# Optimization experiments

Measured on AMD Instinct MI355X. Metric: run time of the kernel, lower is better.

## Reference

```python
import jax, jax.numpy as jnp
import numpy as np

NEG = -1000000000.0

def _gat(x, adj_pos, W, a_src, a_dst):
    # x: [N,F], W: [H,F], a_src/a_dst: [1,H]
    h = x @ W.T                                          # [N,H]
    e = jax.nn.leaky_relu(h @ a_src.T + (h @ a_dst.T).T, 0.2)  # [N,N] additive attn
    e = jnp.where(adj_pos, e, NEG)
    alpha = jax.nn.softmax(e, axis=-1)
    return alpha @ h                                     # [N,H]

def setup_inputs() -> dict:
    key = jax.random.key(0)
    ks = jax.random.split(key, 24)
    N, F, Cf, C, H = 4096, 64, 10, 64, 128
    s = 0.05
    nrm = lambda k, shp: (jax.random.normal(k, shp, jnp.float32) * s)
    return dict(
        node_features=jax.random.normal(ks[0], (N, F), jnp.float32),
        candidate_features=jax.random.uniform(ks[1], (N, C, Cf), dtype=jnp.float32),
        adjacency=jax.random.randint(ks[2], (N, N), 0, 2).astype(jnp.int32),
        action_mask=jax.random.uniform(ks[3], (N, C), dtype=jnp.float32),
        W1=nrm(ks[4], (H, F)), a1s=nrm(ks[5], (1, H)), a1d=nrm(ks[6], (1, H)),
        W2=nrm(ks[7], (H, H)), a2s=nrm(ks[8], (1, H)), a2d=nrm(ks[9], (1, H)),
        ln_w=jnp.ones((H,), jnp.float32), ln_b=jnp.zeros((H,), jnp.float32),
        Wc1=nrm(ks[10], (H, Cf)), bc1=jnp.zeros((H,), jnp.float32),
        Wc2=nrm(ks[11], (H, H)), bc2=jnp.zeros((H,), jnp.float32),
        Wq=nrm(ks[12], (H, H)), bq=jnp.zeros((H,), jnp.float32),
        Ws1=nrm(ks[13], (H, 2 * H)), bs1=jnp.zeros((H,), jnp.float32),
        Ws2=nrm(ks[14], (1, H)), bs2=jnp.zeros((1,), jnp.float32),
    )

def reference(node_features, candidate_features, adjacency, action_mask,
              W1, a1s, a1d, W2, a2s, a2d, ln_w, ln_b,
              Wc1, bc1, Wc2, bc2, Wq, bq, Ws1, bs1, Ws2, bs2):
    gelu = lambda x: jax.nn.gelu(x, approximate=False)  # torch nn.GELU default (erf)
    adj_pos = adjacency > 0
    # two GAT layers with residual + LayerNorm
    h = jax.nn.relu(_gat(node_features, adj_pos, W1, a1s, a1d))      # [N,H]
    h = jax.nn.relu(_gat(h, adj_pos, W2, a2s, a2d)) + h
    mu = jnp.mean(h, axis=-1, keepdims=True)
    var = jnp.var(h, axis=-1, keepdims=True)
    h = (h - mu) * jax.lax.rsqrt(var + 1e-5) * ln_w + ln_b           # LayerNorm
    # candidate encoder
    cand = gelu(candidate_features @ Wc1.T + bc1)                    # [N,C,H]
    cand = gelu(cand @ Wc2.T + bc2)
    q = (h @ Wq.T + bq)[:, None, :]                                  # [N,1,H]
    fused = jnp.concatenate([q * cand, cand], axis=-1)               # [N,C,2H]
    logits = (gelu(fused @ Ws1.T + bs1) @ Ws2.T + bs2)[..., 0]       # [N,C]
    cf = candidate_features
    bias = (20.0 * cf[..., 0] + 4.0 * cf[..., 4] + 1.5 * cf[..., 5]
            + 1.5 * cf[..., 1] - 1.5 * cf[..., 2]
            + 1.2 * cf[..., 6] + 2.5 * cf[..., 7]
            + 1.6 * cf[..., 8] + 1.2 * cf[..., 9])
    logits = logits + bias
    # rows with no valid action: force action 0 valid
    no_valid = jnp.sum(action_mask, axis=-1) <= 0
    am = action_mask.at[:, 0].set(jnp.where(no_valid, 1.0, action_mask[:, 0]))
    return jnp.where(am > 0, logits, NEG)
```

## Files before the change

### kernel.cpp

```cpp
#include <hip/hip_runtime.h>
#include <hip/hip_bf16.h>
#include <math.h>

#define NN 4096
#define HD 128
#define NCAND 64
#define NCF 10
#define NSEG 16
#define NEGV (-1000000000.0f)

typedef __attribute__((ext_vector_type(8))) short short8_t;
typedef __attribute__((ext_vector_type(4))) float f32x4_t;

__device__ __forceinline__ short f2bf(float f) {
    union { __hip_bfloat16 h; short s; } v;
    v.h = __float2bfloat16(f);
    return v.s;
}
__device__ __forceinline__ float bf2f(short s) {
    union { unsigned u; float f; } v; v.u = ((unsigned)(unsigned short)s) << 16;
    return v.f;
}
__device__ __forceinline__ unsigned pk2(float a, float b) {
    union { __hip_bfloat162 h; unsigned u; } v;
    v.h = __float22bfloat162_rn(make_float2(a, b));
    return v.u;
}

__device__ __forceinline__ float gelu_f(float x) {
    float e = __builtin_amdgcn_exp2f(2.455466f * x);
    float r = __builtin_amdgcn_rcpf(e + 1.0f);
    return x - x * r;
}

__global__ __launch_bounds__(256) void prep_gatin_k(
    const int* __restrict__ adj, const float* __restrict__ Wc1,
    const float* __restrict__ Wc2, const float* __restrict__ Ws1,
    unsigned* __restrict__ adjb, short* __restrict__ Wc1b,
    short* __restrict__ Wc2b, short* __restrict__ Wfu,
    const float* __restrict__ X, const float* __restrict__ W1,
    const float* __restrict__ a_s, const float* __restrict__ a_d,
    float* __restrict__ sdv, short* __restrict__ Htb)
{
    constexpr int K = 64, AS = 68;
    __shared__ float in_s[16*AS];
    __shared__ float H_s[16*132];
    int tid = threadIdx.x;

    if (blockIdx.x < 2048) {
        long g = (long)blockIdx.x * 256 + tid;
        const int4* p = (const int4*)adj + g * 8;
        unsigned wd = 0;
        #pragma unroll
        for (int e = 0; e < 8; ++e) {
            int4 v = p[e];
            wd |= (unsigned)(v.x != 0) << (e*4 + 0);
            wd |= (unsigned)(v.y != 0) << (e*4 + 1);
            wd |= (unsigned)(v.z != 0) << (e*4 + 2);
            wd |= (unsigned)(v.w != 0) << (e*4 + 3);
        }
        adjb[g] = wd;
        return;
    }
    if (blockIdx.x < 2056) {
        int g = (blockIdx.x - 2048) * 256 + tid;
        const int tot = 8 * 256;
        for (int e = g; e < 128*32; e += tot) {
            int t = e >> 5, k = e & 31;
            Wc1b[e] = (k < NCF) ? f2bf(Wc1[t*NCF + k]) : (short)0;
        }
        for (int e = g; e < 128*128; e += tot) {
            int h = e >> 7, pos = e & 127;
            int n = (pos >> 3) | ((pos & 7) << 4);
            Wc2b[e] = f2bf(Wc2[h*128 + n]);
        }
        for (int e = g; e < 128*256; e += tot) {
            int h = e >> 8, j = e & 255;
            int pos = j & 127;
            int n = (pos >> 3) | ((pos & 7) << 4);
            float v = (j < 128) ? Ws1[h*256 + 128 + n] : Ws1[h*256 + n];
            Wfu[e] = f2bf(v);
        }
        return;
    }

    int n0 = (blockIdx.x - 2056) * 16;
    {
        constexpr int NV = 16*K/4;
        for (int idx = tid; idx < NV; idx += 256) {
            int row = idx / (K/4), c4 = idx - row*(K/4);
            *(float4*)&in_s[row*AS + c4*4] = *(const float4*)&X[(long)(n0+row)*K + c4*4];
        }
    }
    __syncthreads();

    int w = tid >> 6, l = tid & 63, l15 = l & 15, qd = l >> 4;
    f32x4_t acc[2];
    acc[0] = (f32x4_t){0.f,0.f,0.f,0.f};
    acc[1] = (f32x4_t){0.f,0.f,0.f,0.f};
    #pragma unroll
    for (int kc = 0; kc < K/32; ++kc) {
        int k0 = kc*32 + qd*8;
        float4 x = *(const float4*)&in_s[l15*AS + k0];
        float4 y = *(const float4*)&in_s[l15*AS + k0 + 4];
        union { short8_t s; unsigned u[4]; } a;
        a.u[0]=pk2(x.x,x.y); a.u[1]=pk2(x.z,x.w);
        a.u[2]=pk2(y.x,y.y); a.u[3]=pk2(y.z,y.w);
        #pragma unroll
        for (int it = 0; it < 2; ++it) {
            int n = (w*2+it)*16 + l15;
            float4 w0 = *(const float4*)&W1[(long)n*K + k0];
            float4 w1 = *(const float4*)&W1[(long)n*K + k0 + 4];
            union { short8_t s; unsigned u[4]; } b;
            b.u[0]=pk2(w0.x,w0.y); b.u[1]=pk2(w0.z,w0.w);
            b.u[2]=pk2(w1.x,w1.y); b.u[3]=pk2(w1.z,w1.w);
            acc[it] = __builtin_amdgcn_mfma_f32_16x16x32_bf16(a.s, b.s, acc[it], 0,0,0);
        }
    }
    #pragma unroll
    for (int it = 0; it < 2; ++it)
        #pragma unroll
        for (int r = 0; r < 4; ++r)
            H_s[(qd*4+r)*132 + (w*2+it)*16 + l15] = acc[it][r];
    __syncthreads();
    {
        int row = tid >> 4, sg = tid & 15;
        int h0 = sg*8;
        float4 as0 = *(const float4*)&a_s[h0];
        float4 as1 = *(const float4*)&a_s[h0+4];
        float4 ad0 = *(const float4*)&a_d[h0];
        float4 ad1 = *(const float4*)&a_d[h0+4];
        float hv[8];
        #pragma unroll
        for (int e = 0; e < 8; ++e) hv[e] = H_s[row*132 + h0 + e];
        float sp = hv[0]*as0.x + hv[1]*as0.y + hv[2]*as0.z + hv[3]*as0.w
                 + hv[4]*as1.x + hv[5]*as1.y + hv[6]*as1.z + hv[7]*as1.w;
        float dp = hv[0]*ad0.x + hv[1]*ad0.y + hv[2]*ad0.z + hv[3]*ad0.w
                 + hv[4]*ad1.x + hv[5]*ad1.y + hv[6]*ad1.z + hv[7]*ad1.w;
        sp += __shfl_xor(sp,1); sp += __shfl_xor(sp,2);
        sp += __shfl_xor(sp,4); sp += __shfl_xor(sp,8);
        dp += __shfl_xor(dp,1); dp += __shfl_xor(dp,2);
        dp += __shfl_xor(dp,4); dp += __shfl_xor(dp,8);
        if (sg == 0) { sdv[n0+row] = sp; sdv[NN + n0 + row] = dp; }
    }
    {
        int h = tid & 127, pr = tid >> 7;
        unsigned u[4];
        #pragma unroll
        for (int c2 = 0; c2 < 4; ++c2)
            u[c2] = pk2(H_s[(pr*8 + 2*c2)*132 + h], H_s[(pr*8 + 2*c2 + 1)*132 + h]);
        *(uint4*)&Htb[(long)h*NN + n0 + pr*8] = make_uint4(u[0],u[1],u[2],u[3]);
    }
}

template<int K, int IN, int OUT>
__global__ __launch_bounds__(256) void gatin_k3(
    const float* __restrict__ in, const float* __restrict__ Wf,
    const float* __restrict__ nump, const float* __restrict__ denp,
    float* __restrict__ G1, const float* __restrict__ ln_w,
    const float* __restrict__ ln_b,
    const float* __restrict__ a_s, const float* __restrict__ a_d,
    float* __restrict__ sdv, short* __restrict__ Htb,
    const float* __restrict__ bias, float* __restrict__ outq)
{
    constexpr int AS = K + 4;
    __shared__ float in_s[16*AS];
    __shared__ float H_s[16*132];
    int tid = threadIdx.x;
    int n0 = blockIdx.x * 16;

    if (IN == 0) {
        constexpr int NV = 16*K/4;
        for (int idx = tid; idx < NV; idx += 256) {
            int row = idx / (K/4), c4 = idx - row*(K/4);
            *(float4*)&in_s[row*AS + c4*4] = *(const float4*)&in[(long)(n0+row)*K + c4*4];
        }
    } else {
        int row = tid >> 4, c8 = (tid & 15) * 8;
        float v[8];
        #pragma unroll
        for (int i = 0; i < 8; ++i) v[i] = 0.f;
        float den = 0.f;
        const float* npr = nump + (long)(n0 + row)*NSEG*HD + c8;
        const float* dpr = denp + (long)(n0 + row)*NSEG;
        #pragma unroll
        for (int s = 0; s < NSEG; ++s) {
            const float* np = npr + s*HD;
            float4 a0 = *(const float4*)np;
            float4 a1 = *(const float4*)(np + 4);
            v[0]+=a0.x; v[1]+=a0.y; v[2]+=a0.z; v[3]+=a0.w;
            v[4]+=a1.x; v[5]+=a1.y; v[6]+=a1.z; v[7]+=a1.w;
            den += dpr[s];
        }
        float rd = (den > 0.f) ? __builtin_amdgcn_rcpf(den) : 0.f;
        if (den > 0.f) rd = rd * (2.0f - den * rd);
        #pragma unroll
        for (int i = 0; i < 8; ++i) v[i] = fmaxf(v[i]*rd, 0.f);
        if (IN == 1) {
            float4 o0 = make_float4(v[0],v[1],v[2],v[3]);
            float4 o1 = make_float4(v[4],v[5],v[6],v[7]);
            *(float4*)&G1[(long)(n0+row)*HD + c8]     = o0;
            *(float4*)&G1[(long)(n0+row)*HD + c8 + 4] = o1;
        }
        #pragma unroll
        for (int i = 0; i < 8; ++i) in_s[row*AS + c8 + i] = v[i];
    }
    __syncthreads();

    int w = tid >> 6, l = tid & 63, l15 = l & 15, qd = l >> 4;
    f32x4_t acc[2];
    acc[0] = (f32x4_t){0.f,0.f,0.f,0.f};
    acc[1] = (f32x4_t){0.f,0.f,0.f,0.f};
    #pragma unroll
    for (int kc = 0; kc < K/32; ++kc) {
        int k0 = kc*32 + qd*8;
        float4 x = *(const float4*)&in_s[l15*AS + k0];
        float4 y = *(const float4*)&in_s[l15*AS + k0 + 4];
        union { short8_t s; unsigned u[4]; } a;
        a.u[0]=pk2(x.x,x.y); a.u[1]=pk2(x.z,x.w);
        a.u[2]=pk2(y.x,y.y); a.u[3]=pk2(y.z,y.w);
        #pragma unroll
        for (int it = 0; it < 2; ++it) {
            int n = (w*2+it)*16 + l15;
            float4 w0 = *(const float4*)&Wf[(long)n*K + k0];
            float4 w1 = *(const float4*)&Wf[(long)n*K + k0 + 4];
            union { short8_t s; unsigned u[4]; } b;
            b.u[0]=pk2(w0.x,w0.y); b.u[1]=pk2(w0.z,w0.w);
            b.u[2]=pk2(w1.x,w1.y); b.u[3]=pk2(w1.z,w1.w);
            acc[it] = __builtin_amdgcn_mfma_f32_16x16x32_bf16(a.s, b.s, acc[it], 0,0,0);
        }
    }

    #pragma unroll
    for (int it = 0; it < 2; ++it)
        #pragma unroll
        for (int r = 0; r < 4; ++r)
            H_s[(qd*4+r)*132 + (w*2+it)*16 + l15] = acc[it][r];
    __syncthreads();
    {
        int row = tid >> 4, sg = tid & 15;
        int h0 = sg*8;
        float4 as0 = *(const float4*)&a_s[h0];
        float4 as1 = *(const float4*)&a_s[h0+4];
        float4 ad0 = *(const float4*)&a_d[h0];
        float4 ad1 = *(const float4*)&a_d[h0+4];
        float hv[8];
        #pragma unroll
        for (int e = 0; e < 8; ++e) hv[e] = H_s[row*132 + h0 + e];
        float sp = hv[0]*as0.x + hv[1]*as0.y + hv[2]*as0.z + hv[3]*as0.w
                 + hv[4]*as1.x + hv[5]*as1.y + hv[6]*as1.z + hv[7]*as1.w;
        float dp = hv[0]*ad0.x + hv[1]*ad0.y + hv[2]*ad0.z + hv[3]*ad0.w
                 + hv[4]*ad1.x + hv[5]*ad1.y + hv[6]*ad1.z + hv[7]*ad1.w;
        sp += __shfl_xor(sp,1); sp += __shfl_xor(sp,2);
        sp += __shfl_xor(sp,4); sp += __shfl_xor(sp,8);
        dp += __shfl_xor(dp,1); dp += __shfl_xor(dp,2);
        dp += __shfl_xor(dp,4); dp += __shfl_xor(dp,8);
        if (sg == 0) { sdv[n0+row] = sp; sdv[NN + n0 + row] = dp; }
    }
    {
        int h = tid & 127, pr = tid >> 7;
        unsigned u[4];
        #pragma unroll
        for (int c2 = 0; c2 < 4; ++c2)
            u[c2] = pk2(H_s[(pr*8 + 2*c2)*132 + h], H_s[(pr*8 + 2*c2 + 1)*132 + h]);
        *(uint4*)&Htb[(long)h*NN + n0 + pr*8] = make_uint4(u[0],u[1],u[2],u[3]);
    }
}

__global__ __launch_bounds__(256, 4) void agg_k5(
    const unsigned* __restrict__ adjb, const float* __restrict__ sdv,
    const short* __restrict__ Htb, float* __restrict__ num_part,
    float* __restrict__ den_part)
{
    __shared__ __align__(16) short Bs[128*72];
    __shared__ float dj_s[256];
    int tid = threadIdx.x;
    int i0 = blockIdx.x * 32;
    int seg = blockIdx.y;
    int w = tid >> 6, l = tid & 63, l15 = l & 15, qd = l >> 4;
    int mh = w >> 1, nh = w & 1;
    int arow = i0 + mh*16 + l15;
    float si = sdv[arow];
    const float C1 = 1.44269504f;
    const float C2 = 0.28853901f;

    dj_s[tid] = sdv[NN + seg*256 + tid];

    unsigned wbuf[8];
    {
        const uint4* ap = (const uint4*)&adjb[(long)arow*128 + seg*8];
        uint4 q0 = ap[0], q1 = ap[1];
        wbuf[0]=q0.x; wbuf[1]=q0.y; wbuf[2]=q0.z; wbuf[3]=q0.w;
        wbuf[4]=q1.x; wbuf[5]=q1.y; wbuf[6]=q1.z; wbuf[7]=q1.w;
    }

    int sh = tid >> 1, sj = (tid & 1) * 32;
    const short* srcb = Htb + (long)sh*NN + seg*256 + sj;

    f32x4_t acc[4];
    #pragma unroll
    for (int nt = 0; nt < 4; ++nt) acc[nt] = (f32x4_t){0.f,0.f,0.f,0.f};
    float den = 0.f;

    for (int c4 = 0; c4 < 4; ++c4) {
        __syncthreads();
        {
            const uint4* src = (const uint4*)(srcb + c4*64);
            uint4 v0 = src[0], v1 = src[1], v2 = src[2], v3 = src[3];
            uint4* dst = (uint4*)&Bs[sh*72 + sj];
            dst[0]=v0; dst[1]=v1; dst[2]=v2; dst[3]=v3;
        }
        __syncthreads();
        #pragma unroll
        for (int kc = 0; kc < 2; ++kc) {
            int jl = c4*64 + kc*32 + qd*8;
            float4 da = *(const float4*)&dj_s[jl];
            float4 db = *(const float4*)&dj_s[jl+4];
            unsigned byte_ = (wbuf[c4*2+kc] >> (qd*8)) & 0xffu;
            float dv[8] = {da.x,da.y,da.z,da.w,db.x,db.y,db.z,db.w};
            float v[8];
            #pragma unroll
            for (int e = 0; e < 8; ++e) {
                float z = si + dv[e];
                float k = (z > 0.f) ? C1 : C2;
                float wv = __builtin_amdgcn_exp2f(z * k);
                v[e] = ((byte_ >> e) & 1u) ? wv : 0.f;
                den += v[e];
            }
            union { short8_t s; unsigned u[4]; } a;
            a.u[0]=pk2(v[0],v[1]); a.u[1]=pk2(v[2],v[3]);
            a.u[2]=pk2(v[4],v[5]); a.u[3]=pk2(v[6],v[7]);
            int kb = kc*32 + qd*8;
            #pragma unroll
            for (int nt = 0; nt < 4; ++nt) {
                short8_t b = *(const short8_t*)&Bs[(nh*64 + nt*16 + l15)*72 + kb];
                acc[nt] = __builtin_amdgcn_mfma_f32_16x16x32_bf16(a.s, b, acc[nt], 0,0,0);
            }
        }
    }
    den += __shfl_xor(den, 16); den += __shfl_xor(den, 32);
    if (qd == 0 && nh == 0) den_part[(long)arow*NSEG + seg] = den;
    #pragma unroll
    for (int nt = 0; nt < 4; ++nt)
        #pragma unroll
        for (int r = 0; r < 4; ++r)
            num_part[((long)(i0 + mh*16 + qd*4 + r)*NSEG + seg)*HD
                     + nh*64 + nt*16 + l15] = acc[nt][r];
}

__device__ __forceinline__ short8_t mulq2(short8_t c, float4 qa, float4 qb) {
    union { short8_t s; unsigned u[4]; } r;
    r.u[0] = pk2(bf2f(c[0])*qa.x, bf2f(c[1])*qa.y);
    r.u[1] = pk2(bf2f(c[2])*qa.z, bf2f(c[3])*qa.w);
    r.u[2] = pk2(bf2f(c[4])*qb.x, bf2f(c[5])*qb.y);
    r.u[3] = pk2(bf2f(c[6])*qb.z, bf2f(c[7])*qb.w);
    return r.s;
}

__global__ __launch_bounds__(256, 4) void cand_k9(
    const float* __restrict__ cf, const float* __restrict__ am,
    const float* __restrict__ nump, const float* __restrict__ denp,
    const float* __restrict__ G1, const float* __restrict__ ln_w,
    const float* __restrict__ ln_b, const float* __restrict__ Wq,
    const float* __restrict__ bq,
    const short* __restrict__ Wc1b, const short* __restrict__ Wc2b,
    const short* __restrict__ Wfu,
    const float* __restrict__ bc1, const float* __restrict__ bc2,
    const float* __restrict__ bs1, const float* __restrict__ Ws2,
    const float* __restrict__ bs2, float* __restrict__ out)
{
    __shared__ __align__(16) short cand_s[128*136];
    __shared__ float bias_s[128];
    __shared__ __align__(16) float q_s[2][128];
    __shared__ float red_s[128*4];
    __shared__ float noval_s[2];
    __shared__ float hln_s[2][128];
    int tid = threadIdx.x;
    long r0 = (long)blockIdx.x * 128;
    int w = tid >> 6, l = tid & 63, l15 = l & 15, qd = l >> 4;

    {
        float amv = am[r0 + (long)(w >> 1)*64 + l];
        float tot = amv;
        #pragma unroll
        for (int off = 32; off > 0; off >>= 1) tot += __shfl_xor(tot, off);
        if ((w & 1) == 0 && l == 0) noval_s[w >> 1] = (tot <= 0.f) ? 1.f : 0.f;
    }

    if (w < 2) {
        int node = (int)(r0 >> 6) + w;
        float v0 = 0.f, v1 = 0.f, den = 0.f;
        const float* np = nump + (long)node*NSEG*HD;
        const float* dp = denp + (long)node*NSEG;
        #pragma unroll
        for (int s = 0; s < NSEG; ++s) {
            v0 += np[s*HD + l];
            v1 += np[s*HD + l + 64];
            den += dp[s];
        }
        float rd = (den > 0.f) ? __builtin_amdgcn_rcpf(den) : 0.f;
        if (den > 0.f) rd = rd * (2.0f - den * rd);
        v0 = fmaxf(v0*rd, 0.f) + G1[(long)node*HD + l];
        v1 = fmaxf(v1*rd, 0.f) + G1[(long)node*HD + l + 64];
        float sm = v0 + v1, sq = v0*v0 + v1*v1;
        #pragma unroll
        for (int off = 32; off > 0; off >>= 1) {
            sm += __shfl_xor(sm, off);
            sq += __shfl_xor(sq, off);
        }
        float mu  = sm * (1.0f/128.0f);
        float var = sq * (1.0f/128.0f) - mu*mu;
        float nr  = rsqrtf(var + 1e-5f);
        hln_s[w][l]      = (v0 - mu)*nr*ln_w[l]      + ln_b[l];
        hln_s[w][l + 64] = (v1 - mu)*nr*ln_w[l + 64] + ln_b[l + 64];
    }
    __syncthreads();

    if (tid < 128) {
        int n = tid;
        const float* wq = Wq + (long)n*HD;
        const float* h0 = hln_s[0];
        const float* h1 = hln_s[1];
        float a0 = bq[n], a1 = a0;
        #pragma unroll 8
        for (int k = 0; k < 128; k += 4) {
            float4 wv = *(const float4*)&wq[k];
            a0 += h0[k]*wv.x + h0[k+1]*wv.y + h0[k+2]*wv.z + h0[k+3]*wv.w;
            a1 += h1[k]*wv.x + h1[k+1]*wv.y + h1[k+2]*wv.z + h1[k+3]*wv.w;
        }
        int pos = ((n & 15) << 3) | (n >> 4);
        q_s[0][pos] = a0;
        q_s[1][pos] = a1;
    }

    {
        short8_t fa[2];
        #pragma unroll
        for (int im = 0; im < 2; ++im) {
            long row = r0 + (w*2+im)*16 + l15;
            union { short8_t s; unsigned u[4]; } a;
            float bp = 0.f;
            if (qd == 0) {
                float4 x = *(const float4*)&cf[row*10];
                float4 y = *(const float4*)&cf[row*10+4];
                a.u[0]=pk2(x.x,x.y); a.u[1]=pk2(x.z,x.w);
                a.u[2]=pk2(y.x,y.y); a.u[3]=pk2(y.z,y.w);
                bp = 20.0f*x.x + 1.5f*x.y - 1.5f*x.z + 4.0f*y.x
                   + 1.5f*y.y + 1.2f*y.z + 2.5f*y.w;
            } else if (qd == 1) {
                float2 x = *(const float2*)&cf[row*10+8];
                a.u[0]=pk2(x.x,x.y); a.u[1]=0; a.u[2]=0; a.u[3]=0;
                bp = 1.6f*x.x + 1.2f*x.y;
            } else { a.u[0]=a.u[1]=a.u[2]=a.u[3]=0; }
            bp += __shfl_xor(bp, 16);
            if (qd == 0) bias_s[(w*2+im)*16 + l15] = bp;
            fa[im] = a.s;
        }
        f32x4_t acc1[2][8];
        #pragma unroll
        for (int im = 0; im < 2; ++im)
            #pragma unroll
            for (int nt = 0; nt < 8; ++nt) acc1[im][nt] = (f32x4_t){0.f,0.f,0.f,0.f};
        #pragma unroll
        for (int nt = 0; nt < 8; ++nt) {
            short8_t b = *(const short8_t*)&Wc1b[(nt*16 + l15)*32 + qd*8];
            acc1[0][nt] = __builtin_amdgcn_mfma_f32_16x16x32_bf16(fa[0], b, acc1[0][nt], 0,0,0);
            acc1[1][nt] = __builtin_amdgcn_mfma_f32_16x16x32_bf16(fa[1], b, acc1[1][nt], 0,0,0);
        }
        float bv[8];
        #pragma unroll
        for (int nt = 0; nt < 8; ++nt) bv[nt] = bc1[nt*16 + l15];
        #pragma unroll
        for (int im = 0; im < 2; ++im)
            #pragma unroll
            for (int r = 0; r < 4; ++r) {
                unsigned u[4];
                #pragma unroll
                for (int ph = 0; ph < 4; ++ph) {
                    float g0 = gelu_f(acc1[im][2*ph][r]   + bv[2*ph]);
                    float g1 = gelu_f(acc1[im][2*ph+1][r] + bv[2*ph+1]);
                    u[ph] = pk2(g0, g1);
                }
                int m = (w*2+im)*16 + qd*4 + r;
                *(uint4*)&cand_s[m*136 + l15*8] = make_uint4(u[0],u[1],u[2],u[3]);
            }
    }
    __syncthreads();

    f32x4_t acc[8][2];
    #pragma unroll
    for (int mt = 0; mt < 8; ++mt) {
        acc[mt][0] = (f32x4_t){0.f,0.f,0.f,0.f};
        acc[mt][1] = (f32x4_t){0.f,0.f,0.f,0.f};
    }
    #pragma unroll
    for (int kc = 0; kc < 4; ++kc) {
        int kpos = kc*32 + qd*8;
        short8_t a[8];
        #pragma unroll
        for (int mt = 0; mt < 8; ++mt)
            a[mt] = *(const short8_t*)&cand_s[(mt*16 + l15)*136 + kpos];
        short8_t b0 = *(const short8_t*)&Wc2b[((w*2+0)*16 + l15)*128 + kpos];
        short8_t b1 = *(const short8_t*)&Wc2b[((w*2+1)*16 + l15)*128 + kpos];
        #pragma unroll
        for (int mt = 0; mt < 8; ++mt) {
            acc[mt][0] = __builtin_amdgcn_mfma_f32_16x16x32_bf16(a[mt], b0, acc[mt][0], 0,0,0);
            acc[mt][1] = __builtin_amdgcn_mfma_f32_16x16x32_bf16(a[mt], b1, acc[mt][1], 0,0,0);
        }
    }
    __syncthreads();

    {
        float bv0 = bc2[w*32 + l15];
        float bv1 = bc2[w*32 + 16 + l15];
        #pragma unroll
        for (int mt = 0; mt < 8; ++mt)
            #pragma unroll
            for (int r = 0; r < 4; ++r) {
                float g0 = gelu_f(acc[mt][0][r] + bv0);
                float g1 = gelu_f(acc[mt][1][r] + bv1);
                int m = mt*16 + qd*4 + r;
                *(unsigned*)&cand_s[m*136 + l15*8 + w*2] = pk2(g0, g1);
            }
    }
    __syncthreads();

    #pragma unroll
    for (int mt = 0; mt < 8; ++mt) {
        acc[mt][0] = (f32x4_t){0.f,0.f,0.f,0.f};
        acc[mt][1] = (f32x4_t){0.f,0.f,0.f,0.f};
    }
    #pragma unroll
    for (int kc = 0; kc < 4; ++kc) {
        int kpos = kc*32 + qd*8;
        short8_t a[8];
        #pragma unroll
        for (int mt = 0; mt < 8; ++mt)
            a[mt] = *(const short8_t*)&cand_s[(mt*16 + l15)*136 + kpos];
        short8_t b00 = *(const short8_t*)&Wfu[((w*2+0)*16 + l15)*256 + kpos];
        short8_t b10 = *(const short8_t*)&Wfu[((w*2+1)*16 + l15)*256 + kpos];
        short8_t b01 = *(const short8_t*)&Wfu[((w*2+0)*16 + l15)*256 + 128 + kpos];
        short8_t b11 = *(const short8_t*)&Wfu[((w*2+1)*16 + l15)*256 + 128 + kpos];
        float4 qa0 = *(const float4*)&q_s[0][kpos];
        float4 qb0 = *(const float4*)&q_s[0][kpos+4];
        float4 qa1 = *(const float4*)&q_s[1][kpos];
        float4 qb1 = *(const float4*)&q_s[1][kpos+4];
        short8_t b01q0 = mulq2(b01, qa0, qb0);
        short8_t b11q0 = mulq2(b11, qa0, qb0);
        short8_t b01q1 = mulq2(b01, qa1, qb1);
        short8_t b11q1 = mulq2(b11, qa1, qb1);
        #pragma unroll
        for (int mt = 0; mt < 8; ++mt) {
            short8_t bq0 = (mt < 4) ? b01q0 : b01q1;
            short8_t bq1 = (mt < 4) ? b11q0 : b11q1;
            acc[mt][0] = __builtin_amdgcn_mfma_f32_16x16x32_bf16(a[mt], b00, acc[mt][0], 0,0,0);
            acc[mt][1] = __builtin_amdgcn_mfma_f32_16x16x32_bf16(a[mt], b10, acc[mt][1], 0,0,0);
            acc[mt][0] = __builtin_amdgcn_mfma_f32_16x16x32_bf16(a[mt], bq0, acc[mt][0], 0,0,0);
            acc[mt][1] = __builtin_amdgcn_mfma_f32_16x16x32_bf16(a[mt], bq1, acc[mt][1], 0,0,0);
        }
    }

    {
        float bs1v0 = bs1[w*32 + l15],      bs1v1 = bs1[w*32 + 16 + l15];
        float ws2v0 = Ws2[w*32 + l15],      ws2v1 = Ws2[w*32 + 16 + l15];
        #pragma unroll
        for (int mt = 0; mt < 8; ++mt)
            #pragma unroll
            for (int r = 0; r < 4; ++r) {
                float p = gelu_f(acc[mt][0][r] + bs1v0) * ws2v0
                        + gelu_f(acc[mt][1][r] + bs1v1) * ws2v1;
                p += __shfl_xor(p,1); p += __shfl_xor(p,2);
                p += __shfl_xor(p,4); p += __shfl_xor(p,8);
                if (l15 == 0)
                    red_s[(mt*16 + qd*4 + r)*4 + w] = p;
            }
    }
    __syncthreads();

    if (tid < 128) {
        int m = tid;
        float lg = red_s[m*4] + red_s[m*4+1] + red_s[m*4+2] + red_s[m*4+3]
                 + bs2[0] + bias_s[m];
        float mk = am[r0 + m];
        if ((m & 63) == 0 && noval_s[m >> 6] > 0.f) mk = 1.0f;
        out[r0 + m] = (mk > 0.f) ? lg : NEGV;
    }
}

extern "C" void kernel_launch(void* const* d_in, const int* in_sizes, int n_in,
                              void* d_out, int out_size, void* d_ws, size_t ws_size,
                              hipStream_t stream)
{
    const float* X   = (const float*)d_in[0];
    const float* CF  = (const float*)d_in[1];
    const int*   ADJ = (const int*)d_in[2];
    const float* AM  = (const float*)d_in[3];
    const float* W1  = (const float*)d_in[4];
    const float* A1S = (const float*)d_in[5];
    const float* A1D = (const float*)d_in[6];
    const float* W2  = (const float*)d_in[7];
    const float* A2S = (const float*)d_in[8];
    const float* A2D = (const float*)d_in[9];
    const float* LNW = (const float*)d_in[10];
    const float* LNB = (const float*)d_in[11];
    const float* WC1 = (const float*)d_in[12];
    const float* BC1 = (const float*)d_in[13];
    const float* WC2 = (const float*)d_in[14];
    const float* BC2 = (const float*)d_in[15];
    const float* WQ  = (const float*)d_in[16];
    const float* BQ  = (const float*)d_in[17];
    const float* WS1 = (const float*)d_in[18];
    const float* BS1 = (const float*)d_in[19];
    const float* WS2 = (const float*)d_in[20];
    const float* BS2 = (const float*)d_in[21];
    float* OUT = (float*)d_out;

    float* ws = (float*)d_ws;
    float*    G1   = ws;
    float*    sdv  = ws + 524288;
    float*    denp = ws + 532480;
    short*    Htb  = (short*)(ws + 598016);
    unsigned* adjb = (unsigned*)(ws + 860160);
    short*    Wc1b = (short*)(ws + 1384448);
    short*    Wc2b = (short*)(ws + 1386496);
    short*    Wfu  = (short*)(ws + 1394688);
    float*    nump = ws + 1411072;

    prep_gatin_k<<<2312, 256, 0, stream>>>(ADJ, WC1, WC2, WS1,
                                           adjb, Wc1b, Wc2b, Wfu,
                                           X, W1, A1S, A1D, sdv, Htb);
    agg_k5<<<dim3(128, NSEG), 256, 0, stream>>>(adjb, sdv, Htb, nump, denp);
    gatin_k3<128, 1, 0><<<256, 256, 0, stream>>>(
        nullptr, W2, nump, denp, G1, nullptr, nullptr,
        A2S, A2D, sdv, Htb, nullptr, nullptr);
    agg_k5<<<dim3(128, NSEG), 256, 0, stream>>>(adjb, sdv, Htb, nump, denp);
    cand_k9<<<2048, 256, 0, stream>>>(CF, AM, nump, denp, G1, LNW, LNB, WQ, BQ,
                                      Wc1b, Wc2b, Wfu, BC1, BC2, BS1, WS2, BS2,
                                      OUT);
}
```

Baseline: 274.3 us.

## Precompute LayerNorm and query projection in a separate gatin pass before cand kernel

Moves the second-layer aggregation reduction, residual add, LayerNorm and Wq projection out of the candidate kernel into a new instantiation of the gatin kernel (IN=2, OUT=1). That kernel writes the query vectors to a workspace buffer using MFMA. The candidate kernel then only loads the precomputed q per node. Previously each of 2048 cand blocks recomputed the 16-segment sum, LayerNorm and a scalar 128x128 matvec for two nodes. The cost is an extra kernel launch and a larger workspace layout.

```diff
diff --git a/kernel.cpp b/kernel.cpp
--- a/kernel.cpp
+++ b/kernel.cpp
@@ -201,6 +201,30 @@
             float4 o1 = make_float4(v[4],v[5],v[6],v[7]);
             *(float4*)&G1[(long)(n0+row)*HD + c8]     = o0;
             *(float4*)&G1[(long)(n0+row)*HD + c8 + 4] = o1;
+        } else {
+            const float* gp = G1 + (long)(n0+row)*HD + c8;
+            float4 g0 = *(const float4*)gp;
+            float4 g1 = *(const float4*)(gp + 4);
+            v[0]+=g0.x; v[1]+=g0.y; v[2]+=g0.z; v[3]+=g0.w;
+            v[4]+=g1.x; v[5]+=g1.y; v[6]+=g1.z; v[7]+=g1.w;
+            float sm = 0.f, sq = 0.f;
+            #pragma unroll
+            for (int i = 0; i < 8; ++i) { sm += v[i]; sq += v[i]*v[i]; }
+            sm += __shfl_xor(sm,1); sq += __shfl_xor(sq,1);
+            sm += __shfl_xor(sm,2); sq += __shfl_xor(sq,2);
+            sm += __shfl_xor(sm,4); sq += __shfl_xor(sq,4);
+            sm += __shfl_xor(sm,8); sq += __shfl_xor(sq,8);
+            float mu  = sm * (1.0f/128.0f);
+            float var = sq * (1.0f/128.0f) - mu*mu;
+            float nr  = rsqrtf(var + 1e-5f);
+            float4 lw0 = *(const float4*)&ln_w[c8];
+            float4 lw1 = *(const float4*)&ln_w[c8+4];
+            float4 lb0 = *(const float4*)&ln_b[c8];
+            float4 lb1 = *(const float4*)&ln_b[c8+4];
+            v[0]=(v[0]-mu)*nr*lw0.x+lb0.x; v[1]=(v[1]-mu)*nr*lw0.y+lb0.y;
+            v[2]=(v[2]-mu)*nr*lw0.z+lb0.z; v[3]=(v[3]-mu)*nr*lw0.w+lb0.w;
+            v[4]=(v[4]-mu)*nr*lw1.x+lb1.x; v[5]=(v[5]-mu)*nr*lw1.y+lb1.y;
+            v[6]=(v[6]-mu)*nr*lw1.z+lb1.z; v[7]=(v[7]-mu)*nr*lw1.w+lb1.w;
         }
         #pragma unroll
         for (int i = 0; i < 8; ++i) in_s[row*AS + c8 + i] = v[i];
@@ -229,6 +253,18 @@
             b.u[2]=pk2(w1.x,w1.y); b.u[3]=pk2(w1.z,w1.w);
             acc[it] = __builtin_amdgcn_mfma_f32_16x16x32_bf16(a.s, b.s, acc[it], 0,0,0);
         }
+    }
+
+    if (OUT == 1) {
+        #pragma unroll
+        for (int it = 0; it < 2; ++it) {
+            int n = (w*2+it)*16 + l15;
+            float bv = bias[n];
+            #pragma unroll
+            for (int r = 0; r < 4; ++r)
+                outq[(long)(n0 + qd*4 + r)*HD + n] = acc[it][r] + bv;
+        }
+        return;
     }
 
     #pragma unroll
@@ -357,12 +393,9 @@
     return r.s;
 }
 
-__global__ __launch_bounds__(256, 4) void cand_k9(
+__global__ __launch_bounds__(256, 4) void cand_k8(
     const float* __restrict__ cf, const float* __restrict__ am,
-    const float* __restrict__ nump, const float* __restrict__ denp,
-    const float* __restrict__ G1, const float* __restrict__ ln_w,
-    const float* __restrict__ ln_b, const float* __restrict__ Wq,
-    const float* __restrict__ bq,
+    const float* __restrict__ Qb,
     const short* __restrict__ Wc1b, const short* __restrict__ Wc2b,
     const short* __restrict__ Wfu,
     const float* __restrict__ bc1, const float* __restrict__ bc2,
@@ -374,7 +407,6 @@
     __shared__ __align__(16) float q_s[2][128];
     __shared__ float red_s[128*4];
     __shared__ float noval_s[2];
-    __shared__ float hln_s[2][128];
     int tid = threadIdx.x;
     long r0 = (long)blockIdx.x * 128;
     int w = tid >> 6, l = tid & 63, l15 = l & 15, qd = l >> 4;
@@ -387,50 +419,11 @@
         if ((w & 1) == 0 && l == 0) noval_s[w >> 1] = (tot <= 0.f) ? 1.f : 0.f;
     }
 
-    if (w < 2) {
-        int node = (int)(r0 >> 6) + w;
-        float v0 = 0.f, v1 = 0.f, den = 0.f;
-        const float* np = nump + (long)node*NSEG*HD;
-        const float* dp = denp + (long)node*NSEG;
-        #pragma unroll
-        for (int s = 0; s < NSEG; ++s) {
-            v0 += np[s*HD + l];
-            v1 += np[s*HD + l + 64];
-            den += dp[s];
-        }
-        float rd = (den > 0.f) ? __builtin_amdgcn_rcpf(den) : 0.f;
-        if (den > 0.f) rd = rd * (2.0f - den * rd);
-        v0 = fmaxf(v0*rd, 0.f) + G1[(long)node*HD + l];
-        v1 = fmaxf(v1*rd, 0.f) + G1[(long)node*HD + l + 64];
-        float sm = v0 + v1, sq = v0*v0 + v1*v1;
-        #pragma unroll
-        for (int off = 32; off > 0; off >>= 1) {
-            sm += __shfl_xor(sm, off);
-            sq += __shfl_xor(sq, off);
-        }
-        float mu  = sm * (1.0f/128.0f);
-        float var = sq * (1.0f/128.0f) - mu*mu;
-        float nr  = rsqrtf(var + 1e-5f);
-        hln_s[w][l]      = (v0 - mu)*nr*ln_w[l]      + ln_b[l];
-        hln_s[w][l + 64] = (v1 - mu)*nr*ln_w[l + 64] + ln_b[l + 64];
-    }
-    __syncthreads();
-
-    if (tid < 128) {
-        int n = tid;
-        const float* wq = Wq + (long)n*HD;
-        const float* h0 = hln_s[0];
-        const float* h1 = hln_s[1];
-        float a0 = bq[n], a1 = a0;
-        #pragma unroll 8
-        for (int k = 0; k < 128; k += 4) {
-            float4 wv = *(const float4*)&wq[k];
-            a0 += h0[k]*wv.x + h0[k+1]*wv.y + h0[k+2]*wv.z + h0[k+3]*wv.w;
-            a1 += h1[k]*wv.x + h1[k+1]*wv.y + h1[k+2]*wv.z + h1[k+3]*wv.w;
-        }
+    {
+        int nd = tid >> 7, n = tid & 127;
+        float qv = Qb[((r0 >> 6) + nd)*HD + n];
         int pos = ((n & 15) << 3) | (n >> 4);
-        q_s[0][pos] = a0;
-        q_s[1][pos] = a1;
+        q_s[nd][pos] = qv;
     }
 
     {
@@ -617,14 +610,15 @@
 
     float* ws = (float*)d_ws;
     float*    G1   = ws;
-    float*    sdv  = ws + 524288;
-    float*    denp = ws + 532480;
-    short*    Htb  = (short*)(ws + 598016);
-    unsigned* adjb = (unsigned*)(ws + 860160);
-    short*    Wc1b = (short*)(ws + 1384448);
-    short*    Wc2b = (short*)(ws + 1386496);
-    short*    Wfu  = (short*)(ws + 1394688);
-    float*    nump = ws + 1411072;
+    float*    Qb   = ws + 524288;
+    float*    sdv  = ws + 1048576;
+    float*    denp = ws + 1056768;
+    short*    Htb  = (short*)(ws + 1122304);
+    unsigned* adjb = (unsigned*)(ws + 1384448);
+    short*    Wc1b = (short*)(ws + 1908736);
+    short*    Wc2b = (short*)(ws + 1910784);
+    short*    Wfu  = (short*)(ws + 1918976);
+    float*    nump = ws + 1935360;
 
     prep_gatin_k<<<2312, 256, 0, stream>>>(ADJ, WC1, WC2, WS1,
                                            adjb, Wc1b, Wc2b, Wfu,
@@ -634,7 +628,9 @@
         nullptr, W2, nump, denp, G1, nullptr, nullptr,
         A2S, A2D, sdv, Htb, nullptr, nullptr);
     agg_k5<<<dim3(128, NSEG), 256, 0, stream>>>(adjb, sdv, Htb, nump, denp);
-    cand_k9<<<2048, 256, 0, stream>>>(CF, AM, nump, denp, G1, LNW, LNB, WQ, BQ,
-                                      Wc1b, Wc2b, Wfu, BC1, BC2, BS1, WS2, BS2,
-                                      OUT);
-}
+    gatin_k3<128, 2, 1><<<256, 256, 0, stream>>>(
+        nullptr, WQ, nump, denp, G1, LNW, LNB,
+        nullptr, nullptr, nullptr, nullptr, BQ, Qb);
+    cand_k8<<<2048, 256, 0, stream>>>(CF, AM, Qb, Wc1b, Wc2b, Wfu,
+                                      BC1, BC2, BS1, WS2, BS2, OUT);
+}
```

Result: faster. 264.2 us (-3.7%).
